# Kernel optimization log

Measured on AMD Instinct MI355X. Metric: run time of the kernel, lower is better.

Reference implementation:

```python
import jax, jax.numpy as jnp
import numpy as np

B, S, D = 8, 512, 512
H, DK = 64, 8          # 64 heads hardcoded in SelfAttentiveLBLBiLM
WIDTH = 16             # local window width
NL = 2                 # highway layers
N = S + 2 * WIDTH      # padded sequence length


def setup_inputs() -> dict:
    key = jax.random.key(0)
    ks = jax.random.split(key, 12)
    s = 0.02
    return {
        "inputs": jax.random.normal(ks[0], (B, S, D), jnp.float32),
        "left_pad": jax.random.normal(ks[1], (WIDTH, D), jnp.float32) * s,
        "right_pad": jax.random.normal(ks[2], (WIDTH, D), jnp.float32) * s,
        "l_Wqkv": jax.random.normal(ks[3], (3, D, D), jnp.float32) * s,
        "l_bqkv": jnp.zeros((3, D), jnp.float32),
        "l_Wo": jax.random.normal(ks[4], (D, D), jnp.float32) * s,
        "l_bo": jnp.zeros((D,), jnp.float32),
        "r_Wqkv": jax.random.normal(ks[5], (3, D, D), jnp.float32) * s,
        "r_bqkv": jnp.zeros((3, D), jnp.float32),
        "r_Wo": jax.random.normal(ks[6], (D, D), jnp.float32) * s,
        "r_bo": jnp.zeros((D,), jnp.float32),
        "lhw_W": jax.random.normal(ks[7], (NL, 2 * D, D), jnp.float32) * s,
        "lhw_b": jnp.zeros((NL, 2 * D), jnp.float32),
        "rhw_W": jax.random.normal(ks[8], (NL, 2 * D, D), jnp.float32) * s,
        "rhw_b": jnp.zeros((NL, 2 * D), jnp.float32),
    }


def _masks(n, width):
    i = jnp.arange(n)[:, None]
    j = jnp.arange(n)[None, :]
    # local_mask: triu(k=-width-1) * (1 - triu(k=1)) -> i-width-1 <= j <= i
    left = (j <= i) & (j >= i - width - 1)
    # right mask is the full flip of the left mask
    right = (j >= i) & (j <= i + width + 1)
    return left, right


def _mha(x, Wqkv, bqkv, Wo, bo, mask):
    b, n, d = x.shape
    # torch Linear: y = x @ W.T + b, W is [out, in]
    qkv = jnp.einsum("bnd,tod->tbno", x, Wqkv) + bqkv[:, None, None, :]
    q, k, v = [t.reshape(b, n, H, DK).transpose(0, 2, 1, 3) for t in qkv]
    scores = jnp.einsum("bhqd,bhkd->bhqk", q, k) / jnp.sqrt(jnp.float32(DK))
    scores = jnp.where(mask[None, None], scores, jnp.float32(-1e9))
    p = jax.nn.softmax(scores, axis=-1)
    out = jnp.einsum("bhqk,bhkd->bhqd", p, v)
    out = out.transpose(0, 2, 1, 3).reshape(b, n, d)
    return out @ Wo.T + bo


def _highway(x, Ws, bs):
    for l in range(NL):
        proj = x @ Ws[l].T + bs[l]
        nonlin = jax.nn.relu(proj[..., :D])
        gate = jax.nn.sigmoid(proj[..., D:])
        x = gate * x + (1.0 - gate) * nonlin
    return x


def reference(inputs, left_pad, right_pad, l_Wqkv, l_bqkv, l_Wo, l_bo,
              r_Wqkv, r_bqkv, r_Wo, r_bo, lhw_W, lhw_b, rhw_W, rhw_b):
    b = inputs.shape[0]
    new_inputs = jnp.concatenate(
        [jnp.broadcast_to(left_pad[None], (b, WIDTH, D)), inputs,
         jnp.broadcast_to(right_pad[None], (b, WIDTH, D))], axis=1)  # [B, N, D]
    left_mask, right_mask = _masks(N, WIDTH)
    new_left = _mha(new_inputs, l_Wqkv, l_bqkv, l_Wo, l_bo, left_mask)
    new_right = _mha(new_inputs, r_Wqkv, r_bqkv, r_Wo, r_bo, right_mask)
    # per-step loop indexes position start + width -> slice [WIDTH : WIDTH + S]
    left_out = _highway(new_left[:, WIDTH:WIDTH + S], lhw_W, lhw_b)
    right_out = _highway(new_right[:, WIDTH:WIDTH + S], rhw_W, rhw_b)
    last = jnp.concatenate([left_out, right_out], axis=-1)  # [B, S, 2D]
    all_layers = last[None]  # [1, B, S, 2D] (single layer stacked on dim 0)
    return (all_layers, last)
```

## Files before the change

### kernel.cpp

```cpp
#include <hip/hip_runtime.h>
#include <math.h>

#define B_ 8
#define S_ 512
#define D_ 512
#define WIDTH_ 16
#define NSEQ 544
#define MROWS 4352
#define MOUT 4096
#define OUTHALF 4194304

typedef _Float16 half8 __attribute__((ext_vector_type(8)));
typedef _Float16 half4 __attribute__((ext_vector_type(4)));
typedef float floatx4 __attribute__((ext_vector_type(4)));

#define GLD16(g, l) __builtin_amdgcn_global_load_lds(                          \
    (const __attribute__((address_space(1))) void*)(g),                        \
    (__attribute__((address_space(3))) void*)(l), 16, 0, 0)

__device__ __forceinline__ float sigmoidf_(float x) {
    return 1.f / (1.f + __expf(-x));
}

__global__ __launch_bounds__(256)
void gemm_qkv(const _Float16* __restrict__ A,
              const _Float16* __restrict__ B0, const _Float16* __restrict__ B1,
              const float* __restrict__ bias0, const float* __restrict__ bias1,
              _Float16* __restrict__ C16) {
    const int lda = 512, ldb = 512, ldc = 1536, K = 512;
    __shared__ _Float16 As[128 * 32];
    __shared__ _Float16 Bs[128 * 32];
    const int t    = threadIdx.x;
    const int wave = t >> 6;
    const int lane = t & 63;
    const int bm = blockIdx.y * 128;
    const int bn = blockIdx.x * 128;
    const int z  = blockIdx.z;
    const _Float16* B = z ? B1 : B0;
    const float* bias = z ? bias1 : bias0;
    _Float16* C = C16 + (size_t)z * MROWS * 1536;
    const int wm = (wave & 1) * 64;
    const int wn = (wave >> 1) * 64;

    const int inst = wave * 2;
    const int r0 = inst * 16 + (lane >> 2);
    const int kf = (lane & 3) * 8;

    const _Float16* Ag0 = A + (size_t)(bm + r0) * lda + kf;
    const _Float16* Ag1 = Ag0 + (size_t)16 * lda;
    const _Float16* Bg0 = B + (size_t)(bn + r0) * ldb + kf;
    const _Float16* Bg1 = Bg0 + (size_t)16 * ldb;
    _Float16* As0 = &As[inst * 512];
    _Float16* As1 = As0 + 512;
    _Float16* Bs0 = &Bs[inst * 512];
    _Float16* Bs1 = Bs0 + 512;

    const int fr = lane & 15;
    const int fq = (lane >> 4) * 8;

    floatx4 acc[4][4] = {};

    for (int k0 = 0; k0 < K; k0 += 32) {
        GLD16(Ag0, As0); GLD16(Ag1, As1);
        GLD16(Bg0, Bs0); GLD16(Bg1, Bs1);
        Ag0 += 32; Ag1 += 32; Bg0 += 32; Bg1 += 32;
        __syncthreads();
        half8 af[4], bf[4];
#pragma unroll
        for (int s = 0; s < 4; s++) {
            af[s] = *(const half8*)&As[(wm + s * 16 + fr) * 32 + fq];
            bf[s] = *(const half8*)&Bs[(wn + s * 16 + fr) * 32 + fq];
        }
#pragma unroll
        for (int i = 0; i < 4; i++)
#pragma unroll
            for (int j = 0; j < 4; j++)
                acc[i][j] = __builtin_amdgcn_mfma_f32_16x16x32_f16(
                    af[i], bf[j], acc[i][j], 0, 0, 0);
        __syncthreads();
    }

    const int rq = (lane >> 4) * 4;
    const int cc = lane & 15;
#pragma unroll
    for (int i = 0; i < 4; i++) {
        const int rbase = bm + wm + i * 16 + rq;
#pragma unroll
        for (int j = 0; j < 4; j++) {
            const int col = bn + wn + j * 16 + cc;
            const float bv = bias[col];
#pragma unroll
            for (int r = 0; r < 4; r++)
                C[(size_t)(rbase + r) * ldc + col] = (_Float16)(acc[i][j][r] + bv);
        }
    }
}

__global__ __launch_bounds__(256)
void gemm_wo(const _Float16* __restrict__ Aall,
             const _Float16* __restrict__ B0, const _Float16* __restrict__ B1,
             const float* __restrict__ bias0, const float* __restrict__ bias1,
             _Float16* __restrict__ x16base) {
    const int lda = 512, ldb = 512, K = 512;
    __shared__ _Float16 As[64 * 32];
    __shared__ _Float16 Bs[128 * 32];
    const int t    = threadIdx.x;
    const int wave = t >> 6;
    const int lane = t & 63;
    const int bm = blockIdx.y * 64;
    const int bn = blockIdx.x * 128;
    const int z  = blockIdx.z;
    const _Float16* A = Aall + (size_t)z * MROWS * 512;
    const _Float16* B = z ? B1 : B0;
    const float* bias = z ? bias1 : bias0;
    _Float16* x16 = x16base + (size_t)z * MOUT * 512;

    const int wm = (wave & 1) * 32;
    const int wn = (wave >> 1) * 64;

    const int rA = wave * 16 + (lane >> 2);
    const int rB = wave * 32 + (lane >> 2);
    const int kf = (lane & 3) * 8;

    const _Float16* Ag0 = A + (size_t)(bm + rA) * lda + kf;
    const _Float16* Bg0 = B + (size_t)(bn + rB) * ldb + kf;
    const _Float16* Bg1 = Bg0 + (size_t)16 * ldb;
    _Float16* As0 = &As[wave * 512];
    _Float16* Bs0 = &Bs[wave * 1024];
    _Float16* Bs1 = Bs0 + 512;

    const int fr = lane & 15;
    const int fq = (lane >> 4) * 8;

    floatx4 acc[2][4] = {};

    for (int k0 = 0; k0 < K; k0 += 32) {
        GLD16(Ag0, As0);
        GLD16(Bg0, Bs0); GLD16(Bg1, Bs1);
        Ag0 += 32; Bg0 += 32; Bg1 += 32;
        __syncthreads();
        half8 af[2], bf[4];
#pragma unroll
        for (int s = 0; s < 2; s++)
            af[s] = *(const half8*)&As[(wm + s * 16 + fr) * 32 + fq];
#pragma unroll
        for (int s = 0; s < 4; s++)
            bf[s] = *(const half8*)&Bs[(wn + s * 16 + fr) * 32 + fq];
#pragma unroll
        for (int i = 0; i < 2; i++)
#pragma unroll
            for (int j = 0; j < 4; j++)
                acc[i][j] = __builtin_amdgcn_mfma_f32_16x16x32_f16(
                    af[i], bf[j], acc[i][j], 0, 0, 0);
        __syncthreads();
    }

    const int rq = (lane >> 4) * 4;
    const int cc = lane & 15;
#pragma unroll
    for (int i = 0; i < 2; i++) {
        const int rbase = bm + wm + i * 16 + rq;
#pragma unroll
        for (int r = 0; r < 4; r++) {
            const int row = rbase + r;
            const int b = row / NSEQ;
            const int s = row - b * NSEQ;
            if (s < WIDTH_ || s >= WIDTH_ + S_) continue;
            const int m = b * S_ + s - WIDTH_;
#pragma unroll
            for (int j = 0; j < 4; j++) {
                const int col = bn + wn + j * 16 + cc;
                x16[(size_t)m * 512 + col] = (_Float16)(acc[i][j][r] + bias[col]);
            }
        }
    }
}

__global__ __launch_bounds__(256)
void gemm_hw(const _Float16* __restrict__ x16inbase,
             const _Float16* __restrict__ W0, const _Float16* __restrict__ W1,
             const float* __restrict__ b0, const float* __restrict__ b1,
             _Float16* __restrict__ x16outbase,
             float* __restrict__ outlastbase,
             float* __restrict__ outallbase) {
    const int lda = 512, ldb = 512, K = 512;
    __shared__ _Float16 As[128 * 32];
    __shared__ _Float16 Bn[64 * 32];
    __shared__ _Float16 Bg[64 * 32];
    const int t    = threadIdx.x;
    const int wave = t >> 6;
    const int lane = t & 63;
    const int bm = blockIdx.y * 128;
    const int bn = blockIdx.x * 64;
    const int z  = blockIdx.z;
    const _Float16* A = x16inbase + (size_t)z * MOUT * 512;
    const _Float16* W = z ? W1 : W0;
    const float* bias = z ? b1 : b0;
    _Float16* x16out = x16outbase ? x16outbase + (size_t)z * MOUT * 512 : nullptr;

    const int wm = (wave & 1) * 64;
    const int wn = (wave >> 1) * 32;

    const int rA = wave * 32 + (lane >> 2);
    const int rB = wave * 16 + (lane >> 2);
    const int kf = (lane & 3) * 8;

    const _Float16* Ag0 = A + (size_t)(bm + rA) * lda + kf;
    const _Float16* Ag1 = Ag0 + (size_t)16 * lda;
    const _Float16* Bn0 = W + (size_t)(bn + rB) * ldb + kf;
    const _Float16* Bg0 = W + (size_t)(512 + bn + rB) * ldb + kf;
    _Float16* As0  = &As[wave * 1024];
    _Float16* As1  = As0 + 512;
    _Float16* Bns0 = &Bn[wave * 512];
    _Float16* Bgs0 = &Bg[wave * 512];

    const int fr = lane & 15;
    const int fq = (lane >> 4) * 8;

    floatx4 accn[4][2] = {};
    floatx4 accg[4][2] = {};

    for (int k0 = 0; k0 < K; k0 += 32) {
        GLD16(Ag0, As0); GLD16(Ag1, As1);
        GLD16(Bn0, Bns0);
        GLD16(Bg0, Bgs0);
        Ag0 += 32; Ag1 += 32; Bn0 += 32; Bg0 += 32;
        __syncthreads();
        half8 af[4], bnf[2], bgf[2];
#pragma unroll
        for (int s = 0; s < 4; s++)
            af[s] = *(const half8*)&As[(wm + s * 16 + fr) * 32 + fq];
#pragma unroll
        for (int s = 0; s < 2; s++) {
            bnf[s] = *(const half8*)&Bn[(wn + s * 16 + fr) * 32 + fq];
            bgf[s] = *(const half8*)&Bg[(wn + s * 16 + fr) * 32 + fq];
        }
#pragma unroll
        for (int i = 0; i < 4; i++)
#pragma unroll
            for (int j = 0; j < 2; j++) {
                accn[i][j] = __builtin_amdgcn_mfma_f32_16x16x32_f16(
                    af[i], bnf[j], accn[i][j], 0, 0, 0);
                accg[i][j] = __builtin_amdgcn_mfma_f32_16x16x32_f16(
                    af[i], bgf[j], accg[i][j], 0, 0, 0);
            }
        __syncthreads();
    }

    float* outlast = outlastbase ? outlastbase + z * 512 : nullptr;
    float* outall  = outallbase  ? outallbase  + z * 512 : nullptr;

    const int rq = (lane >> 4) * 4;
    const int cc = lane & 15;
#pragma unroll
    for (int i = 0; i < 4; i++) {
        const int rbase = bm + wm + i * 16 + rq;
#pragma unroll
        for (int j = 0; j < 2; j++) {
            const int col = bn + wn + j * 16 + cc;
            const float bnl = bias[col];
            const float bgt = bias[512 + col];
#pragma unroll
            for (int r = 0; r < 4; r++) {
                const int row = rbase + r;
                const float nl = fmaxf(accn[i][j][r] + bnl, 0.f);
                const float g  = sigmoidf_(accg[i][j][r] + bgt);
                const float xo = (float)A[(size_t)row * 512 + col];
                const float v  = g * xo + (1.f - g) * nl;
                if (x16out) {
                    x16out[(size_t)row * 512 + col] = (_Float16)v;
                } else {
                    outlast[(size_t)row * 1024 + col] = v;
                    outall[(size_t)row * 1024 + col] = v;
                }
            }
        }
    }
}

__global__ __launch_bounds__(256)
void attn_win(const _Float16* __restrict__ qkvall, _Float16* __restrict__ attall) {
    const int dir = blockIdx.y;
    const int dlo = dir ? 0 : -(WIDTH_ + 1);
    const _Float16* qkv = qkvall + (size_t)dir * MROWS * 1536;
    _Float16* att = attall + (size_t)dir * MROWS * 512;
    const int tid = blockIdx.x * 256 + threadIdx.x;
    const int h  = tid & 63;
    const int bi = tid >> 6;
    const int i  = bi % NSEQ;
    const int b  = bi / NSEQ;
    const int j0 = i + dlo;
    const float scale = 0.35355339059327373f;

    const half8 q8 = *(const half8*)(qkv + (size_t)bi * 1536 + h * 8);
    float q[8];
#pragma unroll
    for (int d = 0; d < 8; d++) q[d] = (float)q8[d];

    float s[18];
    float mx = -1e30f;
#pragma unroll
    for (int jj = 0; jj < 18; jj++) {
        const int j = j0 + jj;
        const int jc = j < 0 ? 0 : (j > NSEQ - 1 ? NSEQ - 1 : j);
        const half8 k8 = *(const half8*)(qkv + (size_t)(b * NSEQ + jc) * 1536 + 512 + h * 8);
        float d = 0.f;
#pragma unroll
        for (int dd = 0; dd < 8; dd++) d = fmaf(q[dd], (float)k8[dd], d);
        s[jj] = (j == jc) ? d * scale : -1e30f;
        mx = fmaxf(mx, s[jj]);
    }
    float sum = 0.f;
#pragma unroll
    for (int jj = 0; jj < 18; jj++) { s[jj] = __expf(s[jj] - mx); sum += s[jj]; }
    const float inv = 1.f / sum;

    float o[8] = {};
#pragma unroll
    for (int jj = 0; jj < 18; jj++) {
        const int j = j0 + jj;
        const int jc = j < 0 ? 0 : (j > NSEQ - 1 ? NSEQ - 1 : j);
        const half8 v8 = *(const half8*)(qkv + (size_t)(b * NSEQ + jc) * 1536 + 1024 + h * 8);
        const float p = s[jj];
#pragma unroll
        for (int dd = 0; dd < 8; dd++) o[dd] = fmaf(p, (float)v8[dd], o[dd]);
    }
    half8 o16;
#pragma unroll
    for (int d = 0; d < 8; d++) o16[d] = (_Float16)(o[d] * inv);
    *(half8*)&att[(size_t)bi * 512 + h * 8] = o16;
}

__global__ void prep(const float* __restrict__ lq, const float* __restrict__ rq,
                     const float* __restrict__ lo, const float* __restrict__ ro,
                     const float* __restrict__ lh, const float* __restrict__ rh,
                     _Float16* __restrict__ wdst,
                     const float* __restrict__ inp,
                     const float* __restrict__ lp,
                     const float* __restrict__ rp,
                     _Float16* __restrict__ padX) {
    const int gb = blockIdx.x;
    if (gb < 4096) {
        int idx = gb * 256 + threadIdx.x;
        const float* src; int off;
        if      (idx < 196608) { src = lq; off = idx; }
        else if (idx < 393216) { src = rq; off = idx - 196608; }
        else if (idx < 458752) { src = lo; off = idx - 393216; }
        else if (idx < 524288) { src = ro; off = idx - 458752; }
        else if (idx < 786432) { src = lh; off = idx - 524288; }
        else                   { src = rh; off = idx - 786432; }
        const float4 v = ((const float4*)src)[off];
        half4 h = { (_Float16)v.x, (_Float16)v.y, (_Float16)v.z, (_Float16)v.w };
        ((half4*)wdst)[idx] = h;
    } else {
        int idx = (gb - 4096) * 256 + threadIdx.x;
        const int c4 = idx & 127;
        const int t  = idx >> 7;
        const int n = t % NSEQ;
        const int b = t / NSEQ;
        const float* src;
        if (n < WIDTH_)            src = lp + n * 512;
        else if (n < WIDTH_ + S_)  src = inp + ((size_t)(b * S_ + n - WIDTH_)) * 512;
        else                       src = rp + (n - WIDTH_ - S_) * 512;
        const float4 v = *(const float4*)(src + c4 * 4);
        half4 h = { (_Float16)v.x, (_Float16)v.y, (_Float16)v.z, (_Float16)v.w };
        *(half4*)&padX[(size_t)t * 512 + c4 * 4] = h;
    }
}

extern "C" void kernel_launch(void* const* d_in, const int* in_sizes, int n_in,
                              void* d_out, int out_size, void* d_ws, size_t ws_size,
                              hipStream_t stream) {
    const float* inputs    = (const float*)d_in[0];
    const float* left_pad  = (const float*)d_in[1];
    const float* right_pad = (const float*)d_in[2];
    const float* l_Wqkv = (const float*)d_in[3];
    const float* l_bqkv = (const float*)d_in[4];
    const float* l_Wo   = (const float*)d_in[5];
    const float* l_bo   = (const float*)d_in[6];
    const float* r_Wqkv = (const float*)d_in[7];
    const float* r_bqkv = (const float*)d_in[8];
    const float* r_Wo   = (const float*)d_in[9];
    const float* r_bo   = (const float*)d_in[10];
    const float* lhw_W  = (const float*)d_in[11];
    const float* lhw_b  = (const float*)d_in[12];
    const float* rhw_W  = (const float*)d_in[13];
    const float* rhw_b  = (const float*)d_in[14];

    float* out = (float*)d_out;
    _Float16* h = (_Float16*)d_ws;

    _Float16* padX16 = h;
    _Float16* w16    = h + 2228224;
    _Float16* lqkv16 = w16;
    _Float16* rqkv16 = w16 + 786432;
    _Float16* lWo16  = w16 + 1572864;
    _Float16* rWo16  = w16 + 1835008;
    _Float16* lhw16  = w16 + 2097152;
    _Float16* rhw16  = w16 + 3145728;
    _Float16* qkv16  = h + 6422528;
    _Float16* att16  = h + 19791872;
    _Float16* x16a   = h + 24248320;
    _Float16* x16b   = h + 28442624;

    float* out_all  = out;
    float* out_last = out + OUTHALF;

    prep<<<6272, 256, 0, stream>>>(l_Wqkv, r_Wqkv, l_Wo, r_Wo, lhw_W, rhw_W, w16,
                                   inputs, left_pad, right_pad, padX16);

    gemm_qkv<<<dim3(12, 34, 2), 256, 0, stream>>>(
        padX16, lqkv16, rqkv16, l_bqkv, r_bqkv, qkv16);

    attn_win<<<dim3(MROWS * 64 / 256, 2), 256, 0, stream>>>(qkv16, att16);

    gemm_wo<<<dim3(4, 68, 2), 256, 0, stream>>>(
        att16, lWo16, rWo16, l_bo, r_bo, x16a);

    gemm_hw<<<dim3(8, 32, 2), 256, 0, stream>>>(
        x16a, lhw16, rhw16, lhw_b, rhw_b, x16b, nullptr, nullptr);
    gemm_hw<<<dim3(8, 32, 2), 256, 0, stream>>>(
        x16b, lhw16 + 524288, rhw16 + 524288, lhw_b + 1024, rhw_b + 1024,
        nullptr, out_last, out_all);
}
```

Measured before the change: 218.7 us.

## Double-buffer LDS in all GEMMs, enlarge Wo tile, use fdot2 in attention

The three GEMM kernels now use two LDS buffers, so the next K-slice is loaded asynchronously while MFMAs run on the current one, with a vmcnt wait plus barrier replacing the paired __syncthreads. gemm_wo goes from 64x128 to 128x128 tiles and launches half as many blocks. The attention QK dot product uses packed fp16 fdot2 when the builtin is available. The changes aim to hide global-load latency and cut barrier count, at the cost of doubled LDS use (possibly lower occupancy) and fewer blocks for the Wo GEMM.

```diff
diff --git a/kernel.cpp b/kernel.cpp
--- a/kernel.cpp
+++ b/kernel.cpp
@@ -12,11 +12,25 @@
 
 typedef _Float16 half8 __attribute__((ext_vector_type(8)));
 typedef _Float16 half4 __attribute__((ext_vector_type(4)));
+typedef _Float16 half2_t __attribute__((ext_vector_type(2)));
 typedef float floatx4 __attribute__((ext_vector_type(4)));
+
+#if defined(__has_builtin)
+#if __has_builtin(__builtin_amdgcn_fdot2)
+#define HAS_FDOT2 1
+#endif
+#endif
 
 #define GLD16(g, l) __builtin_amdgcn_global_load_lds(                          \
     (const __attribute__((address_space(1))) void*)(g),                        \
     (__attribute__((address_space(3))) void*)(l), 16, 0, 0)
+
+#define VMCNT0_BAR()                                                           \
+    do {                                                                       \
+        asm volatile("s_waitcnt vmcnt(0)" ::: "memory");                       \
+        __builtin_amdgcn_s_barrier();                                          \
+        asm volatile("" ::: "memory");                                         \
+    } while (0)
 
 __device__ __forceinline__ float sigmoidf_(float x) {
     return 1.f / (1.f + __expf(-x));
@@ -28,8 +42,8 @@
               const float* __restrict__ bias0, const float* __restrict__ bias1,
               _Float16* __restrict__ C16) {
     const int lda = 512, ldb = 512, ldc = 1536, K = 512;
-    __shared__ _Float16 As[128 * 32];
-    __shared__ _Float16 Bs[128 * 32];
+    __shared__ _Float16 As[2][128 * 32];
+    __shared__ _Float16 Bs[2][128 * 32];
     const int t    = threadIdx.x;
     const int wave = t >> 6;
     const int lane = t & 63;
@@ -50,35 +64,60 @@
     const _Float16* Ag1 = Ag0 + (size_t)16 * lda;
     const _Float16* Bg0 = B + (size_t)(bn + r0) * ldb + kf;
     const _Float16* Bg1 = Bg0 + (size_t)16 * ldb;
-    _Float16* As0 = &As[inst * 512];
-    _Float16* As1 = As0 + 512;
-    _Float16* Bs0 = &Bs[inst * 512];
-    _Float16* Bs1 = Bs0 + 512;
+    const int so = inst * 512;
 
     const int fr = lane & 15;
     const int fq = (lane >> 4) * 8;
 
     floatx4 acc[4][4] = {};
 
-    for (int k0 = 0; k0 < K; k0 += 32) {
-        GLD16(Ag0, As0); GLD16(Ag1, As1);
-        GLD16(Bg0, Bs0); GLD16(Bg1, Bs1);
-        Ag0 += 32; Ag1 += 32; Bg0 += 32; Bg1 += 32;
-        __syncthreads();
-        half8 af[4], bf[4];
-#pragma unroll
-        for (int s = 0; s < 4; s++) {
-            af[s] = *(const half8*)&As[(wm + s * 16 + fr) * 32 + fq];
-            bf[s] = *(const half8*)&Bs[(wn + s * 16 + fr) * 32 + fq];
-        }
-#pragma unroll
-        for (int i = 0; i < 4; i++)
-#pragma unroll
-            for (int j = 0; j < 4; j++)
-                acc[i][j] = __builtin_amdgcn_mfma_f32_16x16x32_f16(
-                    af[i], bf[j], acc[i][j], 0, 0, 0);
-        __syncthreads();
-    }
+#define QKV_STAGE(bf_, koff_)                                                  \
+    do {                                                                       \
+        GLD16(Ag0 + (koff_), &As[bf_][so]);                                    \
+        GLD16(Ag1 + (koff_), &As[bf_][so + 512]);                              \
+        GLD16(Bg0 + (koff_), &Bs[bf_][so]);                                    \
+        GLD16(Bg1 + (koff_), &Bs[bf_][so + 512]);                              \
+    } while (0)
+
+    QKV_STAGE(0, 0);
+    VMCNT0_BAR();
+
+    for (int k0 = 0; k0 < K; k0 += 64) {
+        {
+            half8 af[4], bf[4];
+#pragma unroll
+            for (int s = 0; s < 4; s++) {
+                af[s] = *(const half8*)&As[0][(wm + s * 16 + fr) * 32 + fq];
+                bf[s] = *(const half8*)&Bs[0][(wn + s * 16 + fr) * 32 + fq];
+            }
+            QKV_STAGE(1, k0 + 32);
+#pragma unroll
+            for (int i = 0; i < 4; i++)
+#pragma unroll
+                for (int j = 0; j < 4; j++)
+                    acc[i][j] = __builtin_amdgcn_mfma_f32_16x16x32_f16(
+                        af[i], bf[j], acc[i][j], 0, 0, 0);
+            VMCNT0_BAR();
+        }
+        {
+            half8 af[4], bf[4];
+#pragma unroll
+            for (int s = 0; s < 4; s++) {
+                af[s] = *(const half8*)&As[1][(wm + s * 16 + fr) * 32 + fq];
+                bf[s] = *(const half8*)&Bs[1][(wn + s * 16 + fr) * 32 + fq];
+            }
+            const bool more = (k0 + 64) < K;
+            if (more) QKV_STAGE(0, k0 + 64);
+#pragma unroll
+            for (int i = 0; i < 4; i++)
+#pragma unroll
+                for (int j = 0; j < 4; j++)
+                    acc[i][j] = __builtin_amdgcn_mfma_f32_16x16x32_f16(
+                        af[i], bf[j], acc[i][j], 0, 0, 0);
+            if (more) VMCNT0_BAR();
+        }
+    }
+#undef QKV_STAGE
 
     const int rq = (lane >> 4) * 4;
     const int cc = lane & 15;
@@ -102,12 +141,12 @@
              const float* __restrict__ bias0, const float* __restrict__ bias1,
              _Float16* __restrict__ x16base) {
     const int lda = 512, ldb = 512, K = 512;
-    __shared__ _Float16 As[64 * 32];
-    __shared__ _Float16 Bs[128 * 32];
+    __shared__ _Float16 As[2][128 * 32];
+    __shared__ _Float16 Bs[2][128 * 32];
     const int t    = threadIdx.x;
     const int wave = t >> 6;
     const int lane = t & 63;
-    const int bm = blockIdx.y * 64;
+    const int bm = blockIdx.y * 128;
     const int bn = blockIdx.x * 128;
     const int z  = blockIdx.z;
     const _Float16* A = Aall + (size_t)z * MROWS * 512;
@@ -115,50 +154,76 @@
     const float* bias = z ? bias1 : bias0;
     _Float16* x16 = x16base + (size_t)z * MOUT * 512;
 
-    const int wm = (wave & 1) * 32;
+    const int wm = (wave & 1) * 64;
     const int wn = (wave >> 1) * 64;
 
-    const int rA = wave * 16 + (lane >> 2);
-    const int rB = wave * 32 + (lane >> 2);
+    const int inst = wave * 2;
+    const int r0 = inst * 16 + (lane >> 2);
     const int kf = (lane & 3) * 8;
 
-    const _Float16* Ag0 = A + (size_t)(bm + rA) * lda + kf;
-    const _Float16* Bg0 = B + (size_t)(bn + rB) * ldb + kf;
+    const _Float16* Ag0 = A + (size_t)(bm + r0) * lda + kf;
+    const _Float16* Ag1 = Ag0 + (size_t)16 * lda;
+    const _Float16* Bg0 = B + (size_t)(bn + r0) * ldb + kf;
     const _Float16* Bg1 = Bg0 + (size_t)16 * ldb;
-    _Float16* As0 = &As[wave * 512];
-    _Float16* Bs0 = &Bs[wave * 1024];
-    _Float16* Bs1 = Bs0 + 512;
+    const int so = inst * 512;
 
     const int fr = lane & 15;
     const int fq = (lane >> 4) * 8;
 
-    floatx4 acc[2][4] = {};
-
-    for (int k0 = 0; k0 < K; k0 += 32) {
-        GLD16(Ag0, As0);
-        GLD16(Bg0, Bs0); GLD16(Bg1, Bs1);
-        Ag0 += 32; Bg0 += 32; Bg1 += 32;
-        __syncthreads();
-        half8 af[2], bf[4];
-#pragma unroll
-        for (int s = 0; s < 2; s++)
-            af[s] = *(const half8*)&As[(wm + s * 16 + fr) * 32 + fq];
-#pragma unroll
-        for (int s = 0; s < 4; s++)
-            bf[s] = *(const half8*)&Bs[(wn + s * 16 + fr) * 32 + fq];
-#pragma unroll
-        for (int i = 0; i < 2; i++)
-#pragma unroll
-            for (int j = 0; j < 4; j++)
-                acc[i][j] = __builtin_amdgcn_mfma_f32_16x16x32_f16(
-                    af[i], bf[j], acc[i][j], 0, 0, 0);
-        __syncthreads();
-    }
+    floatx4 acc[4][4] = {};
+
+#define WO_STAGE(bf_, koff_)                                                   \
+    do {                                                                       \
+        GLD16(Ag0 + (koff_), &As[bf_][so]);                                    \
+        GLD16(Ag1 + (koff_), &As[bf_][so + 512]);                              \
+        GLD16(Bg0 + (koff_), &Bs[bf_][so]);                                    \
+        GLD16(Bg1 + (koff_), &Bs[bf_][so + 512]);                              \
+    } while (0)
+
+    WO_STAGE(0, 0);
+    VMCNT0_BAR();
+
+    for (int k0 = 0; k0 < K; k0 += 64) {
+        {
+            half8 af[4], bf[4];
+#pragma unroll
+            for (int s = 0; s < 4; s++) {
+                af[s] = *(const half8*)&As[0][(wm + s * 16 + fr) * 32 + fq];
+                bf[s] = *(const half8*)&Bs[0][(wn + s * 16 + fr) * 32 + fq];
+            }
+            WO_STAGE(1, k0 + 32);
+#pragma unroll
+            for (int i = 0; i < 4; i++)
+#pragma unroll
+                for (int j = 0; j < 4; j++)
+                    acc[i][j] = __builtin_amdgcn_mfma_f32_16x16x32_f16(
+                        af[i], bf[j], acc[i][j], 0, 0, 0);
+            VMCNT0_BAR();
+        }
+        {
+            half8 af[4], bf[4];
+#pragma unroll
+            for (int s = 0; s < 4; s++) {
+                af[s] = *(const half8*)&As[1][(wm + s * 16 + fr) * 32 + fq];
+                bf[s] = *(const half8*)&Bs[1][(wn + s * 16 + fr) * 32 + fq];
+            }
+            const bool more = (k0 + 64) < K;
+            if (more) WO_STAGE(0, k0 + 64);
+#pragma unroll
+            for (int i = 0; i < 4; i++)
+#pragma unroll
+                for (int j = 0; j < 4; j++)
+                    acc[i][j] = __builtin_amdgcn_mfma_f32_16x16x32_f16(
+                        af[i], bf[j], acc[i][j], 0, 0, 0);
+            if (more) VMCNT0_BAR();
+        }
+    }
+#undef WO_STAGE
 
     const int rq = (lane >> 4) * 4;
     const int cc = lane & 15;
 #pragma unroll
-    for (int i = 0; i < 2; i++) {
+    for (int i = 0; i < 4; i++) {
         const int rbase = bm + wm + i * 16 + rq;
 #pragma unroll
         for (int r = 0; r < 4; r++) {
@@ -184,9 +249,9 @@
              float* __restrict__ outlastbase,
              float* __restrict__ outallbase) {
     const int lda = 512, ldb = 512, K = 512;
-    __shared__ _Float16 As[128 * 32];
-    __shared__ _Float16 Bn[64 * 32];
-    __shared__ _Float16 Bg[64 * 32];
+    __shared__ _Float16 As[2][128 * 32];
+    __shared__ _Float16 Bn[2][64 * 32];
+    __shared__ _Float16 Bg[2][64 * 32];
     const int t    = threadIdx.x;
     const int wave = t >> 6;
     const int lane = t & 63;
@@ -209,10 +274,8 @@
     const _Float16* Ag1 = Ag0 + (size_t)16 * lda;
     const _Float16* Bn0 = W + (size_t)(bn + rB) * ldb + kf;
     const _Float16* Bg0 = W + (size_t)(512 + bn + rB) * ldb + kf;
-    _Float16* As0  = &As[wave * 1024];
-    _Float16* As1  = As0 + 512;
-    _Float16* Bns0 = &Bn[wave * 512];
-    _Float16* Bgs0 = &Bg[wave * 512];
+    const int soA = wave * 1024;
+    const int soB = wave * 512;
 
     const int fr = lane & 15;
     const int fq = (lane >> 4) * 8;
@@ -220,32 +283,56 @@
     floatx4 accn[4][2] = {};
     floatx4 accg[4][2] = {};
 
-    for (int k0 = 0; k0 < K; k0 += 32) {
-        GLD16(Ag0, As0); GLD16(Ag1, As1);
-        GLD16(Bn0, Bns0);
-        GLD16(Bg0, Bgs0);
-        Ag0 += 32; Ag1 += 32; Bn0 += 32; Bg0 += 32;
-        __syncthreads();
-        half8 af[4], bnf[2], bgf[2];
-#pragma unroll
-        for (int s = 0; s < 4; s++)
-            af[s] = *(const half8*)&As[(wm + s * 16 + fr) * 32 + fq];
-#pragma unroll
-        for (int s = 0; s < 2; s++) {
-            bnf[s] = *(const half8*)&Bn[(wn + s * 16 + fr) * 32 + fq];
-            bgf[s] = *(const half8*)&Bg[(wn + s * 16 + fr) * 32 + fq];
-        }
-#pragma unroll
-        for (int i = 0; i < 4; i++)
-#pragma unroll
-            for (int j = 0; j < 2; j++) {
-                accn[i][j] = __builtin_amdgcn_mfma_f32_16x16x32_f16(
-                    af[i], bnf[j], accn[i][j], 0, 0, 0);
-                accg[i][j] = __builtin_amdgcn_mfma_f32_16x16x32_f16(
-                    af[i], bgf[j], accg[i][j], 0, 0, 0);
-            }
-        __syncthreads();
-    }
+#define HW_STAGE(bf_, koff_)                                                   \
+    do {                                                                       \
+        GLD16(Ag0 + (koff_), &As[bf_][soA]);                                   \
+        GLD16(Ag1 + (koff_), &As[bf_][soA + 512]);                             \
+        GLD16(Bn0 + (koff_), &Bn[bf_][soB]);                                   \
+        GLD16(Bg0 + (koff_), &Bg[bf_][soB]);                                   \
+    } while (0)
+
+#define HW_COMP(bf_)                                                           \
+    do {                                                                       \
+        half8 af[4], bnf[2], bgf[2];                                           \
+        _Pragma("unroll")                                                      \
+        for (int s = 0; s < 4; s++)                                            \
+            af[s] = *(const half8*)&As[bf_][(wm + s * 16 + fr) * 32 + fq];     \
+        _Pragma("unroll")                                                      \
+        for (int s = 0; s < 2; s++) {                                          \
+            bnf[s] = *(const half8*)&Bn[bf_][(wn + s * 16 + fr) * 32 + fq];    \
+            bgf[s] = *(const half8*)&Bg[bf_][(wn + s * 16 + fr) * 32 + fq];    \
+        }                                                                      \
+        if (stage_next) HW_STAGE(bf_ ^ 1, knext);                              \
+        _Pragma("unroll")                                                      \
+        for (int i = 0; i < 4; i++)                                            \
+            _Pragma("unroll")                                                  \
+            for (int j = 0; j < 2; j++) {                                      \
+                accn[i][j] = __builtin_amdgcn_mfma_f32_16x16x32_f16(           \
+                    af[i], bnf[j], accn[i][j], 0, 0, 0);                       \
+                accg[i][j] = __builtin_amdgcn_mfma_f32_16x16x32_f16(           \
+                    af[i], bgf[j], accg[i][j], 0, 0, 0);                       \
+            }                                                                  \
+    } while (0)
+
+    HW_STAGE(0, 0);
+    VMCNT0_BAR();
+
+    for (int k0 = 0; k0 < K; k0 += 64) {
+        {
+            const bool stage_next = true;
+            const int knext = k0 + 32;
+            HW_COMP(0);
+            VMCNT0_BAR();
+        }
+        {
+            const bool stage_next = (k0 + 64) < K;
+            const int knext = k0 + 64;
+            HW_COMP(1);
+            if (stage_next) VMCNT0_BAR();
+        }
+    }
+#undef HW_STAGE
+#undef HW_COMP
 
     float* outlast = outlastbase ? outlastbase + z * 512 : nullptr;
     float* outall  = outallbase  ? outallbase  + z * 512 : nullptr;
@@ -293,9 +380,11 @@
     const float scale = 0.35355339059327373f;
 
     const half8 q8 = *(const half8*)(qkv + (size_t)bi * 1536 + h * 8);
+#if !defined(HAS_FDOT2)
     float q[8];
 #pragma unroll
     for (int d = 0; d < 8; d++) q[d] = (float)q8[d];
+#endif
 
     float s[18];
     float mx = -1e30f;
@@ -305,8 +394,17 @@
         const int jc = j < 0 ? 0 : (j > NSEQ - 1 ? NSEQ - 1 : j);
         const half8 k8 = *(const half8*)(qkv + (size_t)(b * NSEQ + jc) * 1536 + 512 + h * 8);
         float d = 0.f;
+#if defined(HAS_FDOT2)
+#pragma unroll
+        for (int p = 0; p < 4; p++) {
+            half2_t qa = { q8[2 * p], q8[2 * p + 1] };
+            half2_t ka = { k8[2 * p], k8[2 * p + 1] };
+            d = __builtin_amdgcn_fdot2(qa, ka, d, false);
+        }
+#else
 #pragma unroll
         for (int dd = 0; dd < 8; dd++) d = fmaf(q[dd], (float)k8[dd], d);
+#endif
         s[jj] = (j == jc) ? d * scale : -1e30f;
         mx = fmaxf(mx, s[jj]);
     }
@@ -414,7 +512,7 @@
 
     attn_win<<<dim3(MROWS * 64 / 256, 2), 256, 0, stream>>>(qkv16, att16);
 
-    gemm_wo<<<dim3(4, 68, 2), 256, 0, stream>>>(
+    gemm_wo<<<dim3(4, 34, 2), 256, 0, stream>>>(
         att16, lWo16, rWo16, l_bo, r_bo, x16a);
 
     gemm_hw<<<dim3(8, 32, 2), 256, 0, stream>>>(
```

New measurement: 224.6 us. 2.7% more time.

## Double-buffer LDS in all GEMMs and use fdot2 for attention scores

Applied to the files above, without the earlier changes.

Converts the QKV, output-projection and highway GEMM main loops to a two-stage LDS double buffer with explicit vmcnt waits. Loads for tile k+2 are issued while MFMAs on the current tile run, so global load latency overlaps with compute. It also computes the windowed attention Q·K scores with packed fp16 fdot2 instructions instead of converting to fp32 and using scalar FMAs. The changes double LDS usage per block, which can reduce occupancy, and rely on hand-written waitcnt counts matching the number of issued loads.

```diff
diff --git a/kernel.cpp b/kernel.cpp
--- a/kernel.cpp
+++ b/kernel.cpp
@@ -12,11 +12,26 @@
 
 typedef _Float16 half8 __attribute__((ext_vector_type(8)));
 typedef _Float16 half4 __attribute__((ext_vector_type(4)));
+typedef _Float16 half2_t __attribute__((ext_vector_type(2)));
 typedef float floatx4 __attribute__((ext_vector_type(4)));
+
+#if defined(__has_builtin)
+#if __has_builtin(__builtin_amdgcn_fdot2)
+#define HAS_FDOT2 1
+#endif
+#endif
 
 #define GLD16(g, l) __builtin_amdgcn_global_load_lds(                          \
     (const __attribute__((address_space(1))) void*)(g),                        \
     (__attribute__((address_space(3))) void*)(l), 16, 0, 0)
+
+#define WAIT_VM(n)  asm volatile("s_waitcnt vmcnt(" #n ")" ::: "memory")
+#define WAIT_LGKM0() asm volatile("s_waitcnt lgkmcnt(0)" ::: "memory")
+#define BARRIER()                                                              \
+    do {                                                                       \
+        __builtin_amdgcn_s_barrier();                                          \
+        asm volatile("" ::: "memory");                                         \
+    } while (0)
 
 __device__ __forceinline__ float sigmoidf_(float x) {
     return 1.f / (1.f + __expf(-x));
@@ -27,9 +42,9 @@
               const _Float16* __restrict__ B0, const _Float16* __restrict__ B1,
               const float* __restrict__ bias0, const float* __restrict__ bias1,
               _Float16* __restrict__ C16) {
-    const int lda = 512, ldb = 512, ldc = 1536, K = 512;
-    __shared__ _Float16 As[128 * 32];
-    __shared__ _Float16 Bs[128 * 32];
+    const int lda = 512, ldb = 512, ldc = 1536;
+    __shared__ _Float16 As[2][128 * 32];
+    __shared__ _Float16 Bs[2][128 * 32];
     const int t    = threadIdx.x;
     const int wave = t >> 6;
     const int lane = t & 63;
@@ -50,35 +65,47 @@
     const _Float16* Ag1 = Ag0 + (size_t)16 * lda;
     const _Float16* Bg0 = B + (size_t)(bn + r0) * ldb + kf;
     const _Float16* Bg1 = Bg0 + (size_t)16 * ldb;
-    _Float16* As0 = &As[inst * 512];
-    _Float16* As1 = As0 + 512;
-    _Float16* Bs0 = &Bs[inst * 512];
-    _Float16* Bs1 = Bs0 + 512;
+    const int so = inst * 512;
 
     const int fr = lane & 15;
     const int fq = (lane >> 4) * 8;
 
     floatx4 acc[4][4] = {};
 
-    for (int k0 = 0; k0 < K; k0 += 32) {
-        GLD16(Ag0, As0); GLD16(Ag1, As1);
-        GLD16(Bg0, Bs0); GLD16(Bg1, Bs1);
-        Ag0 += 32; Ag1 += 32; Bg0 += 32; Bg1 += 32;
-        __syncthreads();
+#define QKV_STAGE(bf_, koff_)                                                  \
+    do {                                                                       \
+        GLD16(Ag0 + (koff_), &As[bf_][so]);                                    \
+        GLD16(Ag1 + (koff_), &As[bf_][so + 512]);                              \
+        GLD16(Bg0 + (koff_), &Bs[bf_][so]);                                    \
+        GLD16(Bg1 + (koff_), &Bs[bf_][so + 512]);                              \
+    } while (0)
+
+    QKV_STAGE(0, 0);
+    QKV_STAGE(1, 32);
+
+#pragma unroll
+    for (int tt = 0; tt < 16; tt++) {
+        const int c = tt & 1;
+        if (tt == 15) WAIT_VM(0);
+        else          WAIT_VM(4);
+        BARRIER();
         half8 af[4], bf[4];
 #pragma unroll
         for (int s = 0; s < 4; s++) {
-            af[s] = *(const half8*)&As[(wm + s * 16 + fr) * 32 + fq];
-            bf[s] = *(const half8*)&Bs[(wn + s * 16 + fr) * 32 + fq];
-        }
+            af[s] = *(const half8*)&As[c][(wm + s * 16 + fr) * 32 + fq];
+            bf[s] = *(const half8*)&Bs[c][(wn + s * 16 + fr) * 32 + fq];
+        }
+        WAIT_LGKM0();
+        BARRIER();
+        if (tt + 2 < 16) QKV_STAGE(c, (tt + 2) * 32);
 #pragma unroll
         for (int i = 0; i < 4; i++)
 #pragma unroll
             for (int j = 0; j < 4; j++)
                 acc[i][j] = __builtin_amdgcn_mfma_f32_16x16x32_f16(
                     af[i], bf[j], acc[i][j], 0, 0, 0);
-        __syncthreads();
-    }
+    }
+#undef QKV_STAGE
 
     const int rq = (lane >> 4) * 4;
     const int cc = lane & 15;
@@ -101,9 +128,9 @@
              const _Float16* __restrict__ B0, const _Float16* __restrict__ B1,
              const float* __restrict__ bias0, const float* __restrict__ bias1,
              _Float16* __restrict__ x16base) {
-    const int lda = 512, ldb = 512, K = 512;
-    __shared__ _Float16 As[64 * 32];
-    __shared__ _Float16 Bs[128 * 32];
+    const int lda = 512, ldb = 512;
+    __shared__ _Float16 As[2][64 * 32];
+    __shared__ _Float16 Bs[2][128 * 32];
     const int t    = threadIdx.x;
     const int wave = t >> 6;
     const int lane = t & 63;
@@ -125,35 +152,48 @@
     const _Float16* Ag0 = A + (size_t)(bm + rA) * lda + kf;
     const _Float16* Bg0 = B + (size_t)(bn + rB) * ldb + kf;
     const _Float16* Bg1 = Bg0 + (size_t)16 * ldb;
-    _Float16* As0 = &As[wave * 512];
-    _Float16* Bs0 = &Bs[wave * 1024];
-    _Float16* Bs1 = Bs0 + 512;
+    const int soA = wave * 512;
+    const int soB = wave * 1024;
 
     const int fr = lane & 15;
     const int fq = (lane >> 4) * 8;
 
     floatx4 acc[2][4] = {};
 
-    for (int k0 = 0; k0 < K; k0 += 32) {
-        GLD16(Ag0, As0);
-        GLD16(Bg0, Bs0); GLD16(Bg1, Bs1);
-        Ag0 += 32; Bg0 += 32; Bg1 += 32;
-        __syncthreads();
+#define WO_STAGE(bf_, koff_)                                                   \
+    do {                                                                       \
+        GLD16(Ag0 + (koff_), &As[bf_][soA]);                                   \
+        GLD16(Bg0 + (koff_), &Bs[bf_][soB]);                                   \
+        GLD16(Bg1 + (koff_), &Bs[bf_][soB + 512]);                             \
+    } while (0)
+
+    WO_STAGE(0, 0);
+    WO_STAGE(1, 32);
+
+#pragma unroll
+    for (int tt = 0; tt < 16; tt++) {
+        const int c = tt & 1;
+        if (tt == 15) WAIT_VM(0);
+        else          WAIT_VM(3);
+        BARRIER();
         half8 af[2], bf[4];
 #pragma unroll
         for (int s = 0; s < 2; s++)
-            af[s] = *(const half8*)&As[(wm + s * 16 + fr) * 32 + fq];
+            af[s] = *(const half8*)&As[c][(wm + s * 16 + fr) * 32 + fq];
 #pragma unroll
         for (int s = 0; s < 4; s++)
-            bf[s] = *(const half8*)&Bs[(wn + s * 16 + fr) * 32 + fq];
+            bf[s] = *(const half8*)&Bs[c][(wn + s * 16 + fr) * 32 + fq];
+        WAIT_LGKM0();
+        BARRIER();
+        if (tt + 2 < 16) WO_STAGE(c, (tt + 2) * 32);
 #pragma unroll
         for (int i = 0; i < 2; i++)
 #pragma unroll
             for (int j = 0; j < 4; j++)
                 acc[i][j] = __builtin_amdgcn_mfma_f32_16x16x32_f16(
                     af[i], bf[j], acc[i][j], 0, 0, 0);
-        __syncthreads();
-    }
+    }
+#undef WO_STAGE
 
     const int rq = (lane >> 4) * 4;
     const int cc = lane & 15;
@@ -183,10 +223,10 @@
              _Float16* __restrict__ x16outbase,
              float* __restrict__ outlastbase,
              float* __restrict__ outallbase) {
-    const int lda = 512, ldb = 512, K = 512;
-    __shared__ _Float16 As[128 * 32];
-    __shared__ _Float16 Bn[64 * 32];
-    __shared__ _Float16 Bg[64 * 32];
+    const int lda = 512, ldb = 512;
+    __shared__ _Float16 As[2][128 * 32];
+    __shared__ _Float16 Bn[2][64 * 32];
+    __shared__ _Float16 Bg[2][64 * 32];
     const int t    = threadIdx.x;
     const int wave = t >> 6;
     const int lane = t & 63;
@@ -209,10 +249,8 @@
     const _Float16* Ag1 = Ag0 + (size_t)16 * lda;
     const _Float16* Bn0 = W + (size_t)(bn + rB) * ldb + kf;
     const _Float16* Bg0 = W + (size_t)(512 + bn + rB) * ldb + kf;
-    _Float16* As0  = &As[wave * 1024];
-    _Float16* As1  = As0 + 512;
-    _Float16* Bns0 = &Bn[wave * 512];
-    _Float16* Bgs0 = &Bg[wave * 512];
+    const int soA = wave * 1024;
+    const int soB = wave * 512;
 
     const int fr = lane & 15;
     const int fq = (lane >> 4) * 8;
@@ -220,21 +258,35 @@
     floatx4 accn[4][2] = {};
     floatx4 accg[4][2] = {};
 
-    for (int k0 = 0; k0 < K; k0 += 32) {
-        GLD16(Ag0, As0); GLD16(Ag1, As1);
-        GLD16(Bn0, Bns0);
-        GLD16(Bg0, Bgs0);
-        Ag0 += 32; Ag1 += 32; Bn0 += 32; Bg0 += 32;
-        __syncthreads();
+#define HW_STAGE(bf_, koff_)                                                   \
+    do {                                                                       \
+        GLD16(Ag0 + (koff_), &As[bf_][soA]);                                   \
+        GLD16(Ag1 + (koff_), &As[bf_][soA + 512]);                             \
+        GLD16(Bn0 + (koff_), &Bn[bf_][soB]);                                   \
+        GLD16(Bg0 + (koff_), &Bg[bf_][soB]);                                   \
+    } while (0)
+
+    HW_STAGE(0, 0);
+    HW_STAGE(1, 32);
+
+#pragma unroll
+    for (int tt = 0; tt < 16; tt++) {
+        const int c = tt & 1;
+        if (tt == 15) WAIT_VM(0);
+        else          WAIT_VM(4);
+        BARRIER();
         half8 af[4], bnf[2], bgf[2];
 #pragma unroll
         for (int s = 0; s < 4; s++)
-            af[s] = *(const half8*)&As[(wm + s * 16 + fr) * 32 + fq];
+            af[s] = *(const half8*)&As[c][(wm + s * 16 + fr) * 32 + fq];
 #pragma unroll
         for (int s = 0; s < 2; s++) {
-            bnf[s] = *(const half8*)&Bn[(wn + s * 16 + fr) * 32 + fq];
-            bgf[s] = *(const half8*)&Bg[(wn + s * 16 + fr) * 32 + fq];
-        }
+            bnf[s] = *(const half8*)&Bn[c][(wn + s * 16 + fr) * 32 + fq];
+            bgf[s] = *(const half8*)&Bg[c][(wn + s * 16 + fr) * 32 + fq];
+        }
+        WAIT_LGKM0();
+        BARRIER();
+        if (tt + 2 < 16) HW_STAGE(c, (tt + 2) * 32);
 #pragma unroll
         for (int i = 0; i < 4; i++)
 #pragma unroll
@@ -244,8 +296,8 @@
                 accg[i][j] = __builtin_amdgcn_mfma_f32_16x16x32_f16(
                     af[i], bgf[j], accg[i][j], 0, 0, 0);
             }
-        __syncthreads();
-    }
+    }
+#undef HW_STAGE
 
     float* outlast = outlastbase ? outlastbase + z * 512 : nullptr;
     float* outall  = outallbase  ? outallbase  + z * 512 : nullptr;
@@ -293,9 +345,11 @@
     const float scale = 0.35355339059327373f;
 
     const half8 q8 = *(const half8*)(qkv + (size_t)bi * 1536 + h * 8);
+#if !defined(HAS_FDOT2)
     float q[8];
 #pragma unroll
     for (int d = 0; d < 8; d++) q[d] = (float)q8[d];
+#endif
 
     float s[18];
     float mx = -1e30f;
@@ -305,8 +359,17 @@
         const int jc = j < 0 ? 0 : (j > NSEQ - 1 ? NSEQ - 1 : j);
         const half8 k8 = *(const half8*)(qkv + (size_t)(b * NSEQ + jc) * 1536 + 512 + h * 8);
         float d = 0.f;
+#if defined(HAS_FDOT2)
+#pragma unroll
+        for (int p = 0; p < 4; p++) {
+            half2_t qa = { q8[2 * p], q8[2 * p + 1] };
+            half2_t ka = { k8[2 * p], k8[2 * p + 1] };
+            d = __builtin_amdgcn_fdot2(qa, ka, d, false);
+        }
+#else
 #pragma unroll
         for (int dd = 0; dd < 8; dd++) d = fmaf(q[dd], (float)k8[dd], d);
+#endif
         s[jj] = (j == jc) ? d * scale : -1e30f;
         mx = fmaxf(mx, s[jj]);
     }
```

Result: no change. 217.2 us (-0.7%).
